# Kernel optimization log

Measured on AMD Instinct MI355X. Metric: run time of the kernel, lower is better.

## Reference

```python
import jax, jax.numpy as jnp
import numpy as np

WS = 8      # window size
NH = 8      # num heads
ED = 256    # embed dim
HD = ED // NH  # head dim


def conv2d(x, w, b):
    # x: [B,C,H,W], w: [O,I,3,3] (torch OIHW), SAME padding, stride 1
    y = jax.lax.conv_general_dilated(x, w, (1, 1), 'SAME',
                                     dimension_numbers=('NCHW', 'OIHW', 'NCHW'))
    return y + b[None, :, None, None]


def linear(x, w, b):
    # torch Linear: y = x @ W^T + b, w: [out,in]
    return jnp.einsum('bnc,oc->bno', x, w) + b


def window_partition(x, ws):
    B, C, H, W = x.shape
    x = x.reshape(B, C, H // ws, ws, W // ws, ws)
    x = jnp.transpose(x, (0, 2, 4, 3, 5, 1))  # B, H/ws, W/ws, ws, ws, C
    return x.reshape(-1, ws * ws, C)


def window_reverse(win, H, W, ws, C):
    nW = (H // ws) * (W // ws)
    B = win.shape[0] // nW
    x = win.reshape(B, H // ws, W // ws, ws, ws, C)
    x = jnp.transpose(x, (0, 5, 1, 3, 2, 4))
    return x.reshape(B, C, H, W)


def setup_inputs() -> dict:
    key = jax.random.key(0)
    ks = jax.random.split(key, 24)
    s = 0.02
    inp = {
        'xmap': jax.random.normal(ks[0], (4, ED, 256, 256), jnp.float32),
        'xfeat': jax.random.normal(ks[1], (4, 32, 256, 256), jnp.float32),
        'cmap_w': jax.random.normal(ks[2], (ED, ED, 3, 3), jnp.float32) * s,
        'cmap_b': jnp.zeros((ED,), jnp.float32),
        'cfeat_w': jax.random.normal(ks[3], (ED, 32, 3, 3), jnp.float32) * s,
        'cfeat_b': jnp.zeros((ED,), jnp.float32),
        'qxmap_w': jax.random.normal(ks[4], (ED, ED), jnp.float32) * s,
        'qxmap_b': jnp.zeros((ED,), jnp.float32),
        'kxmap_w': jax.random.normal(ks[5], (ED, ED), jnp.float32) * s,
        'kxmap_b': jnp.zeros((ED,), jnp.float32),
        'vxmap_w': jax.random.normal(ks[6], (ED, ED), jnp.float32) * s,
        'vxmap_b': jnp.zeros((ED,), jnp.float32),
        'qxfeat_w': jax.random.normal(ks[7], (ED, ED), jnp.float32) * s,
        'qxfeat_b': jnp.zeros((ED,), jnp.float32),
        'kxfeat_w': jax.random.normal(ks[8], (ED, ED), jnp.float32) * s,
        'kxfeat_b': jnp.zeros((ED,), jnp.float32),
        'proj_w': jax.random.normal(ks[9], (ED, ED), jnp.float32) * s,
        'proj_b': jnp.zeros((ED,), jnp.float32),
        'cout_w': jax.random.normal(ks[10], (ED, ED, 3, 3), jnp.float32) * s,
        'cout_b': jnp.zeros((ED,), jnp.float32),
    }
    return inp


def reference(xmap, xfeat, cmap_w, cmap_b, cfeat_w, cfeat_b,
              qxmap_w, qxmap_b, kxmap_w, kxmap_b, vxmap_w, vxmap_b,
              qxfeat_w, qxfeat_b, kxfeat_w, kxfeat_b,
              proj_w, proj_b, cout_w, cout_b):
    B, C, H, W = xmap.shape  # xfeat matches spatial size -> no interpolate branch
    xmap = conv2d(xmap, cmap_w, cmap_b)
    identity = xmap
    wm = window_partition(xmap, WS)                        # [Bw, N, C]
    wf = window_partition(conv2d(xfeat, cfeat_w, cfeat_b), WS)
    Bw, N, _ = wm.shape

    def heads(t):
        return jnp.transpose(t.reshape(Bw, N, NH, HD), (0, 2, 1, 3))  # [Bw,H,N,D]

    q_m = heads(linear(wm, qxmap_w, qxmap_b))
    k_m = heads(linear(wm, kxmap_w, kxmap_b))
    v_m = heads(linear(wm, vxmap_w, vxmap_b))
    q_f = heads(linear(wf, qxfeat_w, qxfeat_b))
    k_f = heads(linear(wf, kxfeat_w, kxfeat_b))

    q_g = jax.nn.sigmoid(q_f) * q_m
    k_g = jax.nn.sigmoid(k_f) * k_m

    scale = 1.0 / jnp.sqrt(jnp.asarray(HD, q_g.dtype))
    attn = jax.nn.softmax(jnp.einsum('bhnd,bhmd->bhnm', q_g, k_g) * scale, axis=-1)
    out = jnp.einsum('bhnm,bhmd->bhnd', attn, v_m)         # [Bw,H,N,D]
    out = jnp.transpose(out, (0, 2, 1, 3)).reshape(Bw, N, C)
    out = window_reverse(linear(out, proj_w, proj_b), H, W, WS, C)
    return conv2d(out, cout_w, cout_b) + identity
```

## Files before the change

### kernel.cpp

```cpp
#include <hip/hip_runtime.h>
#include <hip/hip_bf16.h>
#include <cstdint>
#include <math.h>

using bf16 = __hip_bfloat16;
typedef __attribute__((ext_vector_type(4))) float f32x4;
typedef __attribute__((ext_vector_type(8))) short s16x8;
typedef __attribute__((ext_vector_type(4))) short s16x4;

#define AS3(p) ((__attribute__((address_space(3))) void *)(p))
#define AS1(p) ((const __attribute__((address_space(1))) void *)(p))

static constexpr int Himg = 256, Wimg = 256, Bimg = 4;
static constexpr int HWimg = Himg * Wimg;
static constexpr int Ttok = Bimg * HWimg;

__device__ __forceinline__ void gld16(bf16* lds, const bf16* g) {
  __builtin_amdgcn_global_load_lds(AS1(g), AS3(lds), 16, 0, 0);
}

__device__ __forceinline__ unsigned short f2u(float f) {
  bf16 b = __float2bfloat16(f);
  unsigned short u; __builtin_memcpy(&u, &b, 2); return u;
}

__device__ __forceinline__ int remap_lin(int bid, int total) {
  return (bid & 7) * (total >> 3) + (bid >> 3);
}
__device__ __forceinline__ void remap_tile(int bid, int total, int NY, int BMv, int& t0, int& n0) {
  int lin = remap_lin(bid, total);
  t0 = (lin / NY) * BMv;
  n0 = (lin % NY) * 128;
}

__global__ void k_zero4k(float* p) {
  p[blockIdx.x * 256 + threadIdx.x] = 0.f;
}

__global__ void k_castf2b(const float* __restrict__ s, bf16* __restrict__ d, int n) {
  int i = blockIdx.x * 256 + threadIdx.x;
  if (i < n) d[i] = __float2bfloat16(s[i]);
}

__global__ void k_copyf(const float* __restrict__ s, float* __restrict__ d, int n) {
  int i = blockIdx.x * 256 + threadIdx.x;
  if (i < n) d[i] = s[i];
}

__global__ void k_permconv(const float* __restrict__ w, bf16* __restrict__ o, int I) {
  int idx = blockIdx.x * 256 + threadIdx.x;
  int tot = 256 * 9 * I;
  if (idx >= tot) return;
  int i   = idx % I;
  int rem = idx / I;
  int tap = rem % 9;
  int oc  = rem / 9;
  o[idx] = __float2bfloat16(w[(oc * I + i) * 9 + tap]);
}

__global__ void k_tohwc(const float* __restrict__ src, bf16* __restrict__ dst, int C) {
  int bh = blockIdx.x;
  int w0 = blockIdx.y * 32;
  int c0 = blockIdx.z * 32;
  int b = bh / Himg, h = bh % Himg;
  __shared__ float tile[32][33];
  int tid = threadIdx.x;
  int x = tid & 31, y = tid >> 5;
  const float* sp = src + (size_t)b * C * HWimg + (size_t)h * Wimg;
#pragma unroll
  for (int p = 0; p < 4; ++p) {
    int cl = y + p * 8;
    tile[cl][x] = sp[(size_t)(c0 + cl) * HWimg + w0 + x];
  }
  __syncthreads();
#pragma unroll
  for (int p = 0; p < 4; ++p) {
    int wl = y + p * 8;
    dst[((size_t)bh * Wimg + w0 + wl) * C + c0 + x] = __float2bfloat16(tile[x][wl]);
  }
}

__global__ void k_tochw(const bf16* __restrict__ src, float* __restrict__ dst) {
  int bh = blockIdx.x, w0 = blockIdx.y * 32, c0 = blockIdx.z * 32;
  int b = bh >> 8, h = bh & 255;
  __shared__ float tile[32][33];
  int tid = threadIdx.x, x = tid & 31, y = tid >> 5;
  const bf16* sp = src + (size_t)bh * Wimg * 256;
#pragma unroll
  for (int p = 0; p < 4; ++p) {
    int wl = y + p * 8;
    tile[wl][x] = __bfloat162float(sp[(size_t)(w0 + wl) * 256 + c0 + x]);
  }
  __syncthreads();
#pragma unroll
  for (int p = 0; p < 4; ++p) {
    int cl = y + p * 8;
    dst[(((size_t)b * 256 + c0 + cl) * Himg + h) * Wimg + w0 + x] = tile[x][cl];
  }
}

template <int TAPS, int EPI>
__global__ void __launch_bounds__(512, 1)
k_gemm8(const bf16* __restrict__ Ain, const bf16* __restrict__ BT,
        const float* __restrict__ bias,
        bf16* __restrict__ outb, int ldo,
        const bf16* __restrict__ ident,
        const bf16* __restrict__ zp)
{
  constexpr int KTOT = TAPS * 256;
  constexpr int NK64 = KTOT / 64;
  constexpr int NI   = NK64 / 2;
  const int t0 = remap_lin(blockIdx.x, gridDim.x) * 256;
  const int tid  = threadIdx.x;
  const int wave = tid >> 6, lane = tid & 63;
  const int wr = wave >> 2, wc = wave & 3;
  const int fr = lane & 15, fq = lane >> 4;

  __shared__ bf16 A0k0[256 * 32];
  __shared__ bf16 A0k1[256 * 32];
  __shared__ bf16 A1k0[256 * 32];
  __shared__ bf16 A1k1[256 * 32];
  __shared__ bf16 B0k0[256 * 32];
  __shared__ bf16 B0k1[256 * 32];
  __shared__ bf16 B1k0[256 * 32];
  __shared__ bf16 B1k1[256 * 32];

  f32x4 acc[8][4] = {};
  s16x8 bfr[4];

  const int slot8 = (fq ^ ((fr >> 1) & 3)) * 8;
  const int aoff  = (wr * 128 + fr) * 32 + slot8;
  const int boff  = (wc * 64 + fr) * 32 + slot8;
  const int ldsl  = (tid & 3) * 8;
  const int scol  = ((tid & 3) ^ ((tid >> 3) & 3)) * 8;
  const int srow  = tid >> 2;

#define STA(DST, KT, U) do {                                                     \
    const int k0_ = (KT) * 64 + (U) * 32;                                        \
    const int tap_ = k0_ >> 8;                                                   \
    const int c0_ = k0_ & 255;                                                   \
    const int dy_ = tap_ / 3 - 1, dx_ = tap_ % 3 - 1;                            \
    _Pragma("unroll") for (int j_ = 0; j_ < 2; ++j_) {                           \
      const int r_ = j_ * 128 + srow;                                            \
      const int t_ = t0 + r_;                                                    \
      const bf16* s_;                                                            \
      if (TAPS == 1) {                                                           \
        s_ = Ain + (size_t)t_ * 256 + k0_ + scol;                                \
      } else {                                                                   \
        const int hh_ = ((t_ >> 8) & 255) + dy_, ww_ = (t_ & 255) + dx_;         \
        const bool v_ = ((unsigned)hh_ < 256u) && ((unsigned)ww_ < 256u);        \
        const long gi_ = (long)t_ + dy_ * Wimg + dx_;                            \
        s_ = v_ ? (Ain + gi_ * 256 + c0_ + scol) : (zp + scol);                  \
      }                                                                          \
      gld16(DST + r_ * 32 + ldsl, s_);                                           \
    }                                                                            \
  } while (0)

#define STB(DST, KT, U) do {                                                     \
    const int k0_ = (KT) * 64 + (U) * 32;                                        \
    _Pragma("unroll") for (int j_ = 0; j_ < 2; ++j_) {                           \
      const int ch_ = j_ * 128 + srow;                                           \
      gld16(DST + ch_ * 32 + ldsl, BT + (size_t)ch_ * KTOT + k0_ + scol);        \
    }                                                                            \
  } while (0)

#define NVM
#define VM4 asm volatile("s_waitcnt vmcnt(4)" ::: "memory")
#define VM0 asm volatile("s_waitcnt vmcnt(0)" ::: "memory")

#define PH(RA, RB, MH, READB, VMSTMT, ...) do {                                  \
    s16x8 af_[4];                                                                \
    _Pragma("unroll") for (int q_ = 0; q_ < 4; ++q_)                             \
      af_[q_] = *(const s16x8*)((RA) + aoff + ((MH) * 4 + q_) * 512);            \
    if (READB) {                                                                 \
      _Pragma("unroll") for (int n_ = 0; n_ < 4; ++n_)                           \
        bfr[n_] = *(const s16x8*)((RB) + boff + n_ * 512);                       \
    }                                                                            \
    __VA_ARGS__;                                                                 \
    VMSTMT;                                                                      \
    __builtin_amdgcn_sched_barrier(0);                                           \
    __builtin_amdgcn_s_barrier();                                                \
    asm volatile("s_waitcnt lgkmcnt(0)" ::: "memory");                           \
    __builtin_amdgcn_sched_barrier(0);                                           \
    __builtin_amdgcn_s_setprio(1);                                               \
    _Pragma("unroll") for (int q_ = 0; q_ < 4; ++q_)                             \
      _Pragma("unroll") for (int n_ = 0; n_ < 4; ++n_)                           \
        acc[(MH) * 4 + q_][n_] = __builtin_amdgcn_mfma_f32_16x16x32_bf16(        \
            af_[q_], bfr[n_], acc[(MH) * 4 + q_][n_], 0, 0, 0);                  \
    __builtin_amdgcn_s_setprio(0);                                               \
  } while (0)

  STA(A0k0, 0, 0); STB(B0k0, 0, 0);
  STA(A0k1, 0, 1); STB(B0k1, 0, 1);
  VM4;
  __builtin_amdgcn_s_barrier();

#pragma unroll 1
  for (int i = 0; i < NI - 1; ++i) {
    const int v = 2 * i + 1, w = 2 * i + 2;
    PH(A0k0, B0k0, 0, 1, NVM, STA(A1k0, v, 0));
    PH(A0k0, B0k0, 1, 0, VM4, STB(B1k0, v, 0));
    PH(A0k1, B0k1, 0, 1, NVM, STA(A1k1, v, 1));
    PH(A0k1, B0k1, 1, 0, VM4, STB(B1k1, v, 1));
    PH(A1k0, B1k0, 0, 1, NVM, STA(A0k0, w, 0));
    PH(A1k0, B1k0, 1, 0, VM4, STB(B0k0, w, 0));
    PH(A1k1, B1k1, 0, 1, NVM, STA(A0k1, w, 1));
    PH(A1k1, B1k1, 1, 0, VM4, STB(B0k1, w, 1));
  }
  {
    const int v = 2 * NI - 1;
    PH(A0k0, B0k0, 0, 1, NVM, STA(A1k0, v, 0));
    PH(A0k0, B0k0, 1, 0, VM4, STB(B1k0, v, 0));
    PH(A0k1, B0k1, 0, 1, NVM, STA(A1k1, v, 1));
    PH(A0k1, B0k1, 1, 0, VM4, STB(B1k1, v, 1));
    PH(A1k0, B1k0, 0, 1, NVM, );
    PH(A1k0, B1k0, 1, 0, VM0, );
    PH(A1k1, B1k1, 0, 1, NVM, );
    PH(A1k1, B1k1, 1, 0, NVM, );
  }
#undef PH
#undef STA
#undef STB
#undef NVM
#undef VM4
#undef VM0

#pragma unroll
  for (int m = 0; m < 8; ++m) {
#pragma unroll
    for (int n = 0; n < 4; ++n) {
      const int col = wc * 64 + n * 16 + fr;
#pragma unroll
      for (int j = 0; j < 4; ++j) {
        const int row = wr * 128 + m * 16 + fq * 4 + j;
        const size_t t = (size_t)t0 + row;
        float v = acc[m][n][j] + bias[col];
        if (EPI == 0) {
          outb[t * ldo + col] = __float2bfloat16(v);
        } else {
          v += __bfloat162float(ident[t * 256 + col]);
          outb[t * 256 + col] = __float2bfloat16(v);
        }
      }
    }
  }
}

template <int CIN, int TAPS, int EPI>
__global__ void __launch_bounds__(256, 2)
k_gemm(const bf16* __restrict__ Ain, const bf16* __restrict__ BT,
       const float* __restrict__ bias,
       bf16* __restrict__ outb, int ldo,
       const bf16* __restrict__ ident,
       const bf16* __restrict__ zp, int NY)
{
  constexpr int KTOT = TAPS * CIN;
  constexpr int NK = KTOT / 32;
  int t0, n0;
  remap_tile(blockIdx.x, gridDim.x, NY, 256, t0, n0);
  const int tid = threadIdx.x;
  const int wave = tid >> 6, lane = tid & 63;
  const int seg = lane & 3;
  const int rr  = lane >> 2;

  __shared__ bf16 sA0[256 * 32];
  __shared__ bf16 sA1[256 * 32];
  __shared__ bf16 sA2[256 * 32];
  __shared__ bf16 sB0[128 * 32];
  __shared__ bf16 sB1[128 * 32];
  __shared__ bf16 sB2[128 * 32];

  f32x4 acc[8][4] = {};

  const int wr = wave >> 1, wc = wave & 1;
  const int fr = lane & 15, fq = lane >> 4;
  const int sseg = (seg ^ ((rr >> 1) & 3)) * 8;
  const int slot = (fq ^ ((fr >> 1) & 3)) * 8;

#define STAGE(WA, WB, KSV) do {                                                 \
    const int k0_ = (KSV) * 32;                                                 \
    const int tap_ = k0_ / CIN;                                                 \
    const int c0_ = k0_ - tap_ * CIN;                                           \
    const int dy_ = tap_ / 3 - 1, dx_ = tap_ % 3 - 1;                           \
    _Pragma("unroll") for (int i_ = 0; i_ < 4; ++i_) {                          \
      const int g_ = i_ * 4 + wave;                                             \
      const int t_ = t0 + g_ * 16 + rr;                                         \
      const bf16* src_;                                                         \
      if (TAPS == 1) {                                                          \
        src_ = Ain + (size_t)t_ * CIN + k0_ + sseg;                             \
      } else {                                                                  \
        const int hh_ = ((t_ >> 8) & 255) + dy_, ww_ = (t_ & 255) + dx_;        \
        const bool v_ = ((unsigned)hh_ < 256u) && ((unsigned)ww_ < 256u);       \
        const long gi_ = (long)t_ + dy_ * Wimg + dx_;                           \
        src_ = v_ ? (Ain + gi_ * CIN + c0_ + sseg) : (zp + sseg);               \
      }                                                                         \
      gld16(WA + g_ * 16 * 32, src_);                                           \
    }                                                                           \
    _Pragma("unroll") for (int i_ = 0; i_ < 2; ++i_) {                          \
      const int g_ = i_ * 4 + wave;                                             \
      gld16(WB + g_ * 16 * 32,                                                  \
            BT + (size_t)(n0 + g_ * 16 + rr) * KTOT + k0_ + sseg);              \
    }                                                                           \
  } while (0)

#define GSTEP(RA, RB, WA, WB, KSV, LASTF) do {                                  \
    if (LASTF) { asm volatile("s_waitcnt vmcnt(0)" ::: "memory"); }             \
    else       { asm volatile("s_waitcnt vmcnt(6)" ::: "memory"); }             \
    __builtin_amdgcn_s_barrier();                                               \
    s16x8 af_[8], bf_[4];                                                       \
    _Pragma("unroll") for (int m_ = 0; m_ < 8; ++m_)                            \
      af_[m_] = *(const s16x8*)(RA + (wr * 128 + m_ * 16 + fr) * 32 + slot);    \
    _Pragma("unroll") for (int n_ = 0; n_ < 4; ++n_)                            \
      bf_[n_] = *(const s16x8*)(RB + (wc * 64 + n_ * 16 + fr) * 32 + slot);     \
    if ((KSV) + 2 < NK) STAGE(WA, WB, (KSV) + 2);                               \
    __builtin_amdgcn_s_setprio(1);                                              \
    _Pragma("unroll") for (int m_ = 0; m_ < 8; ++m_)                            \
      _Pragma("unroll") for (int n_ = 0; n_ < 4; ++n_)                          \
        acc[m_][n_] = __builtin_amdgcn_mfma_f32_16x16x32_bf16(af_[m_], bf_[n_], acc[m_][n_], 0, 0, 0); \
    __builtin_amdgcn_s_setprio(0);                                              \
  } while (0)

  STAGE(sA0, sB0, 0);
  STAGE(sA1, sB1, 1);

  constexpr int NMAIN = ((NK - 1) / 3) * 3;
  int ks = 0;
#pragma unroll 1
  for (; ks < NMAIN; ks += 3) {
    GSTEP(sA0, sB0, sA2, sB2, ks,     false);
    GSTEP(sA1, sB1, sA0, sB0, ks + 1, false);
    GSTEP(sA2, sB2, sA1, sB1, ks + 2, false);
  }
  constexpr int TREM = NK - NMAIN;
  if constexpr (TREM == 3) {
    GSTEP(sA0, sB0, sA2, sB2, NMAIN,     false);
    GSTEP(sA1, sB1, sA0, sB0, NMAIN + 1, false);
    GSTEP(sA2, sB2, sA1, sB1, NMAIN + 2, true);
  } else if constexpr (TREM == 2) {
    GSTEP(sA0, sB0, sA2, sB2, NMAIN,     false);
    GSTEP(sA1, sB1, sA0, sB0, NMAIN + 1, true);
  } else {
    GSTEP(sA0, sB0, sA2, sB2, NMAIN,     true);
  }
#undef GSTEP
#undef STAGE

#pragma unroll
  for (int m = 0; m < 8; ++m) {
#pragma unroll
    for (int n = 0; n < 4; ++n) {
      const int col = n0 + wc * 64 + n * 16 + fr;
#pragma unroll
      for (int j = 0; j < 4; ++j) {
        const int row = wr * 128 + m * 16 + fq * 4 + j;
        const size_t t = (size_t)t0 + row;
        float v = acc[m][n][j] + bias[col];
        if (EPI == 0) {
          outb[t * ldo + col] = __float2bfloat16(v);
        } else {
          v += __bfloat162float(ident[t * 256 + col]);
          outb[t * 256 + col] = __float2bfloat16(v);
        }
      }
    }
  }
}

__global__ void __launch_bounds__(256, 2)
k_gemm_qkv(const bf16* __restrict__ Am, const bf16* __restrict__ Af,
           const bf16* __restrict__ Bm, const bf16* __restrict__ Bf,
           const float* __restrict__ bm, const float* __restrict__ bfi,
           bf16* __restrict__ out)
{
  int t0, n0;
  remap_tile(blockIdx.x, gridDim.x, 4, 128, t0, n0);
  const int tid = threadIdx.x;
  const int wave = tid >> 6, lane = tid & 63;
  const int seg = lane & 3;
  const int rr  = lane >> 2;

  __shared__ bf16 sA0[128 * 32];
  __shared__ bf16 sA1[128 * 32];
  __shared__ bf16 sA2[128 * 32];
  __shared__ bf16 sB0[128 * 32];
  __shared__ bf16 sB1[128 * 32];
  __shared__ bf16 sB2[128 * 32];

  f32x4 accm[4][4] = {};
  f32x4 accf[4][4] = {};

  const int wr = wave >> 1, wc = wave & 1;
  const int fr = lane & 15, fq = lane >> 4;
  const int sseg = (seg ^ ((rr >> 1) & 3)) * 8;
  const int slot = (fq ^ ((fr >> 1) & 3)) * 8;

#define STAGEQ(WA, WB, SV) do {                                                 \
    const int k0_ = ((SV) >> 1) * 32;                                           \
    const bf16* A_ = ((SV) & 1) ? Af : Am;                                      \
    const bf16* B_ = ((SV) & 1) ? Bf : Bm;                                      \
    _Pragma("unroll") for (int i_ = 0; i_ < 2; ++i_) {                          \
      const int r_ = wave * 32 + i_ * 16 + rr;                                  \
      gld16(WA + (wave * 32 + i_ * 16) * 32, A_ + (size_t)(t0 + r_) * 256 + k0_ + sseg); \
      gld16(WB + (wave * 32 + i_ * 16) * 32, B_ + (size_t)(n0 + r_) * 256 + k0_ + sseg); \
    }                                                                           \
  } while (0)

#define QSTEP(RA, RB, WA, WB, SV, LASTF) do {                                   \
    if (LASTF) { asm volatile("s_waitcnt vmcnt(0)" ::: "memory"); }             \
    else       { asm volatile("s_waitcnt vmcnt(4)" ::: "memory"); }             \
    __builtin_amdgcn_s_barrier();                                               \
    s16x8 af_[4], bf_[4];                                                       \
    _Pragma("unroll") for (int m_ = 0; m_ < 4; ++m_)                            \
      af_[m_] = *(const s16x8*)(RA + (wr * 64 + m_ * 16 + fr) * 32 + slot);     \
    _Pragma("unroll") for (int n_ = 0; n_ < 4; ++n_)                            \
      bf_[n_] = *(const s16x8*)(RB + (wc * 64 + n_ * 16 + fr) * 32 + slot);     \
    if ((SV) + 2 < 16) STAGEQ(WA, WB, (SV) + 2);                                \
    __builtin_amdgcn_s_setprio(1);                                              \
    if ((SV) & 1) {                                                             \
      _Pragma("unroll") for (int m_ = 0; m_ < 4; ++m_)                          \
        _Pragma("unroll") for (int n_ = 0; n_ < 4; ++n_)                        \
          accf[m_][n_] = __builtin_amdgcn_mfma_f32_16x16x32_bf16(af_[m_], bf_[n_], accf[m_][n_], 0, 0, 0); \
    } else {                                                                    \
      _Pragma("unroll") for (int m_ = 0; m_ < 4; ++m_)                          \
        _Pragma("unroll") for (int n_ = 0; n_ < 4; ++n_)                        \
          accm[m_][n_] = __builtin_amdgcn_mfma_f32_16x16x32_bf16(af_[m_], bf_[n_], accm[m_][n_], 0, 0, 0); \
    }                                                                           \
    __builtin_amdgcn_s_setprio(0);                                              \
  } while (0)

  STAGEQ(sA0, sB0, 0);
  STAGEQ(sA1, sB1, 1);

  int s = 0;
#pragma unroll 1
  for (; s < 15; s += 3) {
    QSTEP(sA0, sB0, sA2, sB2, s,     false);
    QSTEP(sA1, sB1, sA0, sB0, s + 1, false);
    QSTEP(sA2, sB2, sA1, sB1, s + 2, false);
  }
  QSTEP(sA0, sB0, sA2, sB2, 15, true);
#undef QSTEP
#undef STAGEQ

#pragma unroll
  for (int m = 0; m < 4; ++m) {
#pragma unroll
    for (int n = 0; n < 4; ++n) {
      const int col = n0 + wc * 64 + n * 16 + fr;
#pragma unroll
      for (int j = 0; j < 4; ++j) {
        const int row = wr * 64 + m * 16 + fq * 4 + j;
        const size_t t = (size_t)t0 + row;
        float v = accm[m][n][j] + bm[col];
        const float g = accf[m][n][j] + bfi[col];
        v *= 1.f / (1.f + __expf(-g));
        out[t * 768 + col] = __float2bfloat16(v);
      }
    }
  }
}

__global__ void __launch_bounds__(256, 2)
k_attn_mfma(const bf16* __restrict__ qkv, bf16* __restrict__ out) {
  __shared__ short smem[4 * 7424];
  const int tid = threadIdx.x;
  const int wave = tid >> 6, lane = tid & 63;
  const int fr = lane & 15, fq = lane >> 4;
  const int wi = blockIdx.x >> 1;
  const int head = (blockIdx.x & 1) * 4 + wave;
  const int b = wi >> 10, rem = wi & 1023, wh = rem >> 5, ww = rem & 31;
  const size_t tbase = (size_t)b * HWimg + (size_t)(wh * 8) * Wimg + ww * 8;

  short* Qs = smem + wave * 7424;
  short* Ks = Qs + 2560;
  short* VT = Qs + 5120;
  short* P  = Qs;
  short* Ol = Qs;

  auto tok = [&](int i) -> size_t {
    return tbase + (size_t)(i >> 3) * Wimg + (i & 7);
  };

  {
    const bf16* tb = qkv + tok(lane) * 768 + head * 32;
#pragma unroll
    for (int c = 0; c < 4; ++c) {
      s16x8 qv = *(const s16x8*)(tb + c * 8);
      s16x8 kv = *(const s16x8*)(tb + 256 + c * 8);
      s16x8 vv = *(const s16x8*)(tb + 512 + c * 8);
      *(s16x8*)(Qs + lane * 40 + c * 8) = qv;
      *(s16x8*)(Ks + lane * 40 + c * 8) = kv;
#pragma unroll
      for (int e = 0; e < 8; ++e) VT[(c * 8 + e) * 72 + lane] = vv[e];
    }
  }

  s16x8 kf[4], qf[4];
#pragma unroll
  for (int m = 0; m < 4; ++m)
    kf[m] = *(const s16x8*)(Ks + (fr + 16 * m) * 40 + fq * 8);
#pragma unroll
  for (int n = 0; n < 4; ++n)
    qf[n] = *(const s16x8*)(Qs + (fr + 16 * n) * 40 + fq * 8);

  f32x4 st[4][4] = {};
#pragma unroll
  for (int m = 0; m < 4; ++m)
#pragma unroll
    for (int n = 0; n < 4; ++n)
      st[m][n] = __builtin_amdgcn_mfma_f32_16x16x32_bf16(kf[m], qf[n], st[m][n], 0, 0, 0);

  const float scale = 0.17677669529663688f;
  float invs[4];
#pragma unroll
  for (int n = 0; n < 4; ++n) {
    float mx = -1e30f;
#pragma unroll
    for (int m = 0; m < 4; ++m)
#pragma unroll
      for (int j = 0; j < 4; ++j) mx = fmaxf(mx, st[m][n][j]);
    mx = fmaxf(mx, __shfl_xor(mx, 16));
    mx = fmaxf(mx, __shfl_xor(mx, 32));
    float sum = 0.f;
#pragma unroll
    for (int m = 0; m < 4; ++m) {
      s16x4 pk;
#pragma unroll
      for (int j = 0; j < 4; ++j) {
        float e = __expf((st[m][n][j] - mx) * scale);
        sum += e;
        pk[j] = (short)f2u(e);
      }
      *(s16x4*)(P + (fr + 16 * n) * 72 + 16 * m + 4 * fq) = pk;
    }
    sum += __shfl_xor(sum, 16);
    sum += __shfl_xor(sum, 32);
    invs[n] = 1.f / sum;
  }

  f32x4 oc[4][2] = {};
#pragma unroll
  for (int ks = 0; ks < 2; ++ks) {
    s16x8 pf[4], vf[2];
#pragma unroll
    for (int m = 0; m < 4; ++m)
      pf[m] = *(const s16x8*)(P + (fr + 16 * m) * 72 + ks * 32 + fq * 8);
#pragma unroll
    for (int n = 0; n < 2; ++n)
      vf[n] = *(const s16x8*)(VT + (fr + 16 * n) * 72 + ks * 32 + fq * 8);
#pragma unroll
    for (int m = 0; m < 4; ++m)
#pragma unroll
      for (int n = 0; n < 2; ++n)
        oc[m][n] = __builtin_amdgcn_mfma_f32_16x16x32_bf16(pf[m], vf[n], oc[m][n], 0, 0, 0);
  }

#pragma unroll
  for (int m = 0; m < 4; ++m)
#pragma unroll
    for (int j = 0; j < 4; ++j) {
      const float inv = __shfl(invs[m], 4 * fq + j);
      const int q = 16 * m + 4 * fq + j;
#pragma unroll
      for (int n = 0; n < 2; ++n)
        Ol[q * 40 + fr + 16 * n] = (short)f2u(oc[m][n][j] * inv);
    }
  {
    bf16* op = out + tok(lane) * 256 + head * 32;
#pragma unroll
    for (int c = 0; c < 4; ++c)
      *(s16x8*)(op + c * 8) = *(const s16x8*)(Ol + lane * 40 + c * 8);
  }
}

extern "C" void kernel_launch(void* const* d_in, const int* in_sizes, int n_in,
                              void* d_out, int out_size, void* d_ws, size_t ws_size,
                              hipStream_t stream) {
  const float* xmap    = (const float*)d_in[0];
  const float* xfeat   = (const float*)d_in[1];
  const float* cmap_w  = (const float*)d_in[2];
  const float* cmap_b  = (const float*)d_in[3];
  const float* cfeat_w = (const float*)d_in[4];
  const float* cfeat_b = (const float*)d_in[5];
  const float* qxmap_w = (const float*)d_in[6];
  const float* qxmap_b = (const float*)d_in[7];
  const float* kxmap_w = (const float*)d_in[8];
  const float* kxmap_b = (const float*)d_in[9];
  const float* vxmap_w = (const float*)d_in[10];
  const float* vxmap_b = (const float*)d_in[11];
  const float* qxfeat_w = (const float*)d_in[12];
  const float* qxfeat_b = (const float*)d_in[13];
  const float* kxfeat_w = (const float*)d_in[14];
  const float* kxfeat_b = (const float*)d_in[15];
  const float* proj_w  = (const float*)d_in[16];
  const float* proj_b  = (const float*)d_in[17];
  const float* cout_w  = (const float*)d_in[18];
  const float* cout_b  = (const float*)d_in[19];

  uint8_t* ws = (uint8_t*)d_ws;
  size_t off = 0;
  auto alloc = [&](size_t bytes) -> void* {
    void* p = ws + off;
    off += (bytes + 255) & ~(size_t)255;
    return p;
  };
  float* zp       = (float*)alloc(4096);
  bf16* cmap_wT   = (bf16*)alloc((size_t)2304 * 256 * 2);
  bf16* cout_wT   = (bf16*)alloc((size_t)2304 * 256 * 2);
  bf16* cfeat_wT  = (bf16*)alloc((size_t)288 * 256 * 2);
  bf16* lin_qkv_wT= (bf16*)alloc((size_t)768 * 256 * 2);
  bf16* lin_f_wT  = (bf16*)alloc((size_t)512 * 256 * 2);
  bf16* proj_wT   = (bf16*)alloc((size_t)256 * 256 * 2);
  float* bias_qkv = (float*)alloc(768 * 4);
  float* bias_f   = (float*)alloc(512 * 4);
  bf16* xm_nhwc   = (bf16*)alloc((size_t)Ttok * 256 * 2);
  bf16* xf_nhwc   = (bf16*)alloc((size_t)Ttok * 32 * 2);
  bf16* xc        = (bf16*)alloc((size_t)Ttok * 256 * 2);
  bf16* fc        = (bf16*)alloc((size_t)Ttok * 256 * 2);
  bf16* qkv       = (bf16*)alloc((size_t)Ttok * 768 * 2);
  bf16* attn_out  = xm_nhwc;
  bf16* proj_out  = fc;
  bf16* convout   = qkv;
  bf16* zpb = (bf16*)zp;

  k_zero4k<<<4, 256, 0, stream>>>(zp);
  k_permconv<<<(256 * 9 * 256 + 255) / 256, 256, 0, stream>>>(cmap_w, cmap_wT, 256);
  k_permconv<<<(256 * 9 * 256 + 255) / 256, 256, 0, stream>>>(cout_w, cout_wT, 256);
  k_permconv<<<(256 * 9 * 32 + 255) / 256, 256, 0, stream>>>(cfeat_w, cfeat_wT, 32);
  k_castf2b<<<256, 256, 0, stream>>>(qxmap_w, lin_qkv_wT, 65536);
  k_castf2b<<<256, 256, 0, stream>>>(kxmap_w, lin_qkv_wT + 65536, 65536);
  k_castf2b<<<256, 256, 0, stream>>>(vxmap_w, lin_qkv_wT + 131072, 65536);
  k_castf2b<<<256, 256, 0, stream>>>(qxfeat_w, lin_f_wT, 65536);
  k_castf2b<<<256, 256, 0, stream>>>(kxfeat_w, lin_f_wT + 65536, 65536);
  k_castf2b<<<256, 256, 0, stream>>>(proj_w, proj_wT, 65536);
  k_copyf<<<1, 256, 0, stream>>>(qxmap_b, bias_qkv, 256);
  k_copyf<<<1, 256, 0, stream>>>(kxmap_b, bias_qkv + 256, 256);
  k_copyf<<<1, 256, 0, stream>>>(vxmap_b, bias_qkv + 512, 256);
  k_copyf<<<1, 256, 0, stream>>>(qxfeat_b, bias_f, 256);
  k_copyf<<<1, 256, 0, stream>>>(kxfeat_b, bias_f + 256, 256);

  k_tohwc<<<dim3(Bimg * Himg, Wimg / 32, 256 / 32), 256, 0, stream>>>(xmap, xm_nhwc, 256);
  k_tohwc<<<dim3(Bimg * Himg, Wimg / 32, 1), 256, 0, stream>>>(xfeat, xf_nhwc, 32);

  const int NB = Ttok / 256;
  k_gemm8<9, 0><<<dim3(NB), dim3(512), 0, stream>>>(
      xm_nhwc, cmap_wT, cmap_b, xc, 256, nullptr, zpb);
  k_gemm<32, 9, 0><<<dim3(NB * 2), dim3(256), 0, stream>>>(
      xf_nhwc, cfeat_wT, cfeat_b, fc, 256, nullptr, zpb, 2);
  k_gemm8<1, 0><<<dim3(NB), dim3(512), 0, stream>>>(
      xc, lin_qkv_wT + 131072, bias_qkv + 512, qkv + 512, 768, nullptr, zpb);
  k_gemm_qkv<<<dim3((Ttok / 128) * 4), dim3(256), 0, stream>>>(
      xc, fc, lin_qkv_wT, lin_f_wT, bias_qkv, bias_f, qkv);
  k_attn_mfma<<<dim3(4096 * 2), dim3(256), 0, stream>>>(qkv, attn_out);
  k_gemm8<1, 0><<<dim3(NB), dim3(512), 0, stream>>>(
      attn_out, proj_wT, proj_b, proj_out, 256, nullptr, zpb);
  k_gemm8<9, 2><<<dim3(NB), dim3(512), 0, stream>>>(
      proj_out, cout_wT, cout_b, convout, 256, xc, zpb);
  k_tochw<<<dim3(Bimg * Himg, Wimg / 32, 256 / 32), 256, 0, stream>>>(convout, (float*)d_out);
}
```

Measured before the change: 1.519 ms.

## Restructure conv GEMM k-loop per tap with hoisted pointers and fewer barriers

The 3x3 conv GEMM main loop now iterates once per filter tap. Per-row A source pointers, including zero-pad selection, are computed once per tap with a lookahead, instead of recomputing address and bounds math on every load. Half of the pipeline phases drop the workgroup s_barrier and keep only the LDS wait, which cuts synchronisation overhead. The risk is LDS read/write hazards if the remaining barriers do not fully protect the double-buffer reuse, along with larger unrolled code.

```diff
diff --git a/kernel.cpp b/kernel.cpp
--- a/kernel.cpp
+++ b/kernel.cpp
@@ -108,8 +108,6 @@
         const bf16* __restrict__ zp)
 {
   constexpr int KTOT = TAPS * 256;
-  constexpr int NK64 = KTOT / 64;
-  constexpr int NI   = NK64 / 2;
   const int t0 = remap_lin(blockIdx.x, gridDim.x) * 256;
   const int tid  = threadIdx.x;
   const int wave = tid >> 6, lane = tid & 63;
@@ -135,40 +133,56 @@
   const int scol  = ((tid & 3) ^ ((tid >> 3) & 3)) * 8;
   const int srow  = tid >> 2;
 
-#define STA(DST, KT, U) do {                                                     \
-    const int k0_ = (KT) * 64 + (U) * 32;                                        \
-    const int tap_ = k0_ >> 8;                                                   \
-    const int c0_ = k0_ & 255;                                                   \
-    const int dy_ = tap_ / 3 - 1, dx_ = tap_ % 3 - 1;                            \
-    _Pragma("unroll") for (int j_ = 0; j_ < 2; ++j_) {                           \
-      const int r_ = j_ * 128 + srow;                                            \
-      const int t_ = t0 + r_;                                                    \
-      const bf16* s_;                                                            \
-      if (TAPS == 1) {                                                           \
-        s_ = Ain + (size_t)t_ * 256 + k0_ + scol;                                \
-      } else {                                                                   \
-        const int hh_ = ((t_ >> 8) & 255) + dy_, ww_ = (t_ & 255) + dx_;         \
-        const bool v_ = ((unsigned)hh_ < 256u) && ((unsigned)ww_ < 256u);        \
-        const long gi_ = (long)t_ + dy_ * Wimg + dx_;                            \
-        s_ = v_ ? (Ain + gi_ * 256 + c0_ + scol) : (zp + scol);                  \
-      }                                                                          \
-      gld16(DST + r_ * 32 + ldsl, s_);                                           \
-    }                                                                            \
+  const bf16* Bb0 = BT + (size_t)srow * KTOT + scol;
+  const bf16* Bb1 = BT + (size_t)(128 + srow) * KTOT + scol;
+  const bf16* Aa0 = Ain + (size_t)(t0 + srow) * 256 + scol;
+  const bf16* Aa1 = Ain + (size_t)(t0 + 128 + srow) * 256 + scol;
+  const bf16 *a0c = Aa0, *a1c = Aa1, *a0n = Aa0, *a1n = Aa1;
+  const int hU = (t0 >> 8) & 255;
+
+  auto mkbase = [&](int tap, const bf16*& o0, const bf16*& o1) {
+    const int dy = tap / 3 - 1, dx = tap % 3 - 1;
+    const bool rowok = ((unsigned)(hU + dy)) < 256u;
+    const long gb = (long)t0 + dy * Wimg + dx;
+    o0 = (rowok && (unsigned)(srow + dx) < 256u)
+             ? Ain + (gb + srow) * 256 + scol : zp + scol;
+    o1 = (rowok && (unsigned)(128 + srow + dx) < 256u)
+             ? Ain + (gb + 128 + srow) * 256 + scol : zp + scol;
+  };
+
+#define STA8(DST, P0, P1, CE) do {                                              \
+    gld16(DST + srow * 32 + ldsl, (P0) + (CE));                                 \
+    gld16(DST + (128 + srow) * 32 + ldsl, (P1) + (CE));                         \
   } while (0)
-
-#define STB(DST, KT, U) do {                                                     \
-    const int k0_ = (KT) * 64 + (U) * 32;                                        \
-    _Pragma("unroll") for (int j_ = 0; j_ < 2; ++j_) {                           \
-      const int ch_ = j_ * 128 + srow;                                           \
-      gld16(DST + ch_ * 32 + ldsl, BT + (size_t)ch_ * KTOT + k0_ + scol);        \
-    }                                                                            \
+#define STB8(DST, KE) do {                                                      \
+    gld16(DST + srow * 32 + ldsl, Bb0 + (KE));                                  \
+    gld16(DST + (128 + srow) * 32 + ldsl, Bb1 + (KE));                          \
   } while (0)
 
-#define NVM
+#define NVMs
 #define VM4 asm volatile("s_waitcnt vmcnt(4)" ::: "memory")
 #define VM0 asm volatile("s_waitcnt vmcnt(0)" ::: "memory")
 
-#define PH(RA, RB, MH, READB, VMSTMT, ...) do {                                  \
+#define PHO(RA, RB, MH, READB, ...) do {                                         \
+    s16x8 af_[4];                                                                \
+    _Pragma("unroll") for (int q_ = 0; q_ < 4; ++q_)                             \
+      af_[q_] = *(const s16x8*)((RA) + aoff + ((MH) * 4 + q_) * 512);            \
+    if (READB) {                                                                 \
+      _Pragma("unroll") for (int n_ = 0; n_ < 4; ++n_)                           \
+        bfr[n_] = *(const s16x8*)((RB) + boff + n_ * 512);                       \
+    }                                                                            \
+    __VA_ARGS__;                                                                 \
+    asm volatile("s_waitcnt lgkmcnt(0)" ::: "memory");                           \
+    __builtin_amdgcn_sched_barrier(0);                                           \
+    __builtin_amdgcn_s_setprio(1);                                               \
+    _Pragma("unroll") for (int q_ = 0; q_ < 4; ++q_)                             \
+      _Pragma("unroll") for (int n_ = 0; n_ < 4; ++n_)                           \
+        acc[(MH) * 4 + q_][n_] = __builtin_amdgcn_mfma_f32_16x16x32_bf16(        \
+            af_[q_], bfr[n_], acc[(MH) * 4 + q_][n_], 0, 0, 0);                  \
+    __builtin_amdgcn_s_setprio(0);                                               \
+  } while (0)
+
+#define PHE(RA, RB, MH, READB, VMSTMT, ...) do {                                 \
     s16x8 af_[4];                                                                \
     _Pragma("unroll") for (int q_ = 0; q_ < 4; ++q_)                             \
       af_[q_] = *(const s16x8*)((RA) + aoff + ((MH) * 4 + q_) * 512);            \
@@ -190,38 +204,78 @@
     __builtin_amdgcn_s_setprio(0);                                               \
   } while (0)
 
-  STA(A0k0, 0, 0); STB(B0k0, 0, 0);
-  STA(A0k1, 0, 1); STB(B0k1, 0, 1);
-  VM4;
-  __builtin_amdgcn_s_barrier();
-
+  if constexpr (TAPS == 9) {
+    mkbase(0, a0c, a1c);
+    mkbase(1, a0n, a1n);
+    STA8(A0k0, a0c, a1c, 0);  STB8(B0k0, 0);
+    STA8(A0k1, a0c, a1c, 32); STB8(B0k1, 32);
+    VM4;
+    __builtin_amdgcn_s_barrier();
 #pragma unroll 1
-  for (int i = 0; i < NI - 1; ++i) {
-    const int v = 2 * i + 1, w = 2 * i + 2;
-    PH(A0k0, B0k0, 0, 1, NVM, STA(A1k0, v, 0));
-    PH(A0k0, B0k0, 1, 0, VM4, STB(B1k0, v, 0));
-    PH(A0k1, B0k1, 0, 1, NVM, STA(A1k1, v, 1));
-    PH(A0k1, B0k1, 1, 0, VM4, STB(B1k1, v, 1));
-    PH(A1k0, B1k0, 0, 1, NVM, STA(A0k0, w, 0));
-    PH(A1k0, B1k0, 1, 0, VM4, STB(B0k0, w, 0));
-    PH(A1k1, B1k1, 0, 1, NVM, STA(A0k1, w, 1));
-    PH(A1k1, B1k1, 1, 0, VM4, STB(B0k1, w, 1));
-  }
-  {
-    const int v = 2 * NI - 1;
-    PH(A0k0, B0k0, 0, 1, NVM, STA(A1k0, v, 0));
-    PH(A0k0, B0k0, 1, 0, VM4, STB(B1k0, v, 0));
-    PH(A0k1, B0k1, 0, 1, NVM, STA(A1k1, v, 1));
-    PH(A0k1, B0k1, 1, 0, VM4, STB(B1k1, v, 1));
-    PH(A1k0, B1k0, 0, 1, NVM, );
-    PH(A1k0, B1k0, 1, 0, VM0, );
-    PH(A1k1, B1k1, 0, 1, NVM, );
-    PH(A1k1, B1k1, 1, 0, NVM, );
-  }
-#undef PH
-#undef STA
-#undef STB
-#undef NVM
+    for (int tap = 0; tap < 8; ++tap) {
+      PHO(A0k0, B0k0, 0, 1, STA8(A1k0, a0c, a1c, 64));
+      PHE(A0k0, B0k0, 1, 0, VM4, STB8(B1k0, 64));
+      PHO(A0k1, B0k1, 0, 1, STA8(A1k1, a0c, a1c, 96));
+      PHE(A0k1, B0k1, 1, 0, VM4, STB8(B1k1, 96));
+      PHO(A1k0, B1k0, 0, 1, STA8(A0k0, a0c, a1c, 128));
+      PHE(A1k0, B1k0, 1, 0, VM4, STB8(B0k0, 128));
+      PHO(A1k1, B1k1, 0, 1, STA8(A0k1, a0c, a1c, 160));
+      PHE(A1k1, B1k1, 1, 0, VM4, STB8(B0k1, 160));
+      PHO(A0k0, B0k0, 0, 1, STA8(A1k0, a0c, a1c, 192));
+      PHE(A0k0, B0k0, 1, 0, VM4, STB8(B1k0, 192));
+      PHO(A0k1, B0k1, 0, 1, STA8(A1k1, a0c, a1c, 224));
+      PHE(A0k1, B0k1, 1, 0, VM4, STB8(B1k1, 224));
+      PHO(A1k0, B1k0, 0, 1, STA8(A0k0, a0n, a1n, 0));
+      PHE(A1k0, B1k0, 1, 0, VM4, STB8(B0k0, 256));
+      PHO(A1k1, B1k1, 0, 1, STA8(A0k1, a0n, a1n, 32));
+      PHE(A1k1, B1k1, 1, 0, VM4, STB8(B0k1, 288));
+      a0c = a0n; a1c = a1n;
+      if (tap + 2 < 9) mkbase(tap + 2, a0n, a1n);
+      Bb0 += 256; Bb1 += 256;
+    }
+    PHO(A0k0, B0k0, 0, 1, STA8(A1k0, a0c, a1c, 64));
+    PHE(A0k0, B0k0, 1, 0, VM4, STB8(B1k0, 64));
+    PHO(A0k1, B0k1, 0, 1, STA8(A1k1, a0c, a1c, 96));
+    PHE(A0k1, B0k1, 1, 0, VM4, STB8(B1k1, 96));
+    PHO(A1k0, B1k0, 0, 1, STA8(A0k0, a0c, a1c, 128));
+    PHE(A1k0, B1k0, 1, 0, VM4, STB8(B0k0, 128));
+    PHO(A1k1, B1k1, 0, 1, STA8(A0k1, a0c, a1c, 160));
+    PHE(A1k1, B1k1, 1, 0, VM4, STB8(B0k1, 160));
+    PHO(A0k0, B0k0, 0, 1, STA8(A1k0, a0c, a1c, 192));
+    PHE(A0k0, B0k0, 1, 0, VM4, STB8(B1k0, 192));
+    PHO(A0k1, B0k1, 0, 1, STA8(A1k1, a0c, a1c, 224));
+    PHE(A0k1, B0k1, 1, 0, VM4, STB8(B1k1, 224));
+    PHO(A1k0, B1k0, 0, 1, );
+    PHE(A1k0, B1k0, 1, 0, VM0, );
+    PHO(A1k1, B1k1, 0, 1, );
+    PHE(A1k1, B1k1, 1, 0, NVMs, );
+  } else {
+    STA8(A0k0, Aa0, Aa1, 0);  STB8(B0k0, 0);
+    STA8(A0k1, Aa0, Aa1, 32); STB8(B0k1, 32);
+    VM4;
+    __builtin_amdgcn_s_barrier();
+    PHO(A0k0, B0k0, 0, 1, STA8(A1k0, Aa0, Aa1, 64));
+    PHE(A0k0, B0k0, 1, 0, VM4, STB8(B1k0, 64));
+    PHO(A0k1, B0k1, 0, 1, STA8(A1k1, Aa0, Aa1, 96));
+    PHE(A0k1, B0k1, 1, 0, VM4, STB8(B1k1, 96));
+    PHO(A1k0, B1k0, 0, 1, STA8(A0k0, Aa0, Aa1, 128));
+    PHE(A1k0, B1k0, 1, 0, VM4, STB8(B0k0, 128));
+    PHO(A1k1, B1k1, 0, 1, STA8(A0k1, Aa0, Aa1, 160));
+    PHE(A1k1, B1k1, 1, 0, VM4, STB8(B0k1, 160));
+    PHO(A0k0, B0k0, 0, 1, STA8(A1k0, Aa0, Aa1, 192));
+    PHE(A0k0, B0k0, 1, 0, VM4, STB8(B1k0, 192));
+    PHO(A0k1, B0k1, 0, 1, STA8(A1k1, Aa0, Aa1, 224));
+    PHE(A0k1, B0k1, 1, 0, VM4, STB8(B1k1, 224));
+    PHO(A1k0, B1k0, 0, 1, );
+    PHE(A1k0, B1k0, 1, 0, VM0, );
+    PHO(A1k1, B1k1, 0, 1, );
+    PHE(A1k1, B1k1, 1, 0, NVMs, );
+  }
+#undef PHO
+#undef PHE
+#undef STA8
+#undef STB8
+#undef NVMs
 #undef VM4
 #undef VM0
 
```

Result: no change. 1.515 ms (median of 2 runs) (-0.2%).
